# Optimization experiments

Hardware: AMD Instinct MI355X
Metric: run time of the kernel (lower is better)

The kernel has to match this reference:

```python
import jax, jax.numpy as jnp
import numpy as np

E = 8      # num_expert
D = 1024   # d_model
H = 2048   # expert hidden (htoh4 size)
K = 2      # top_k
N = 2048   # tokens (batch*seq)


def setup_inputs() -> dict:
    key = jax.random.key(0)
    ks = jax.random.split(key, 4)
    sc = lambda k, shape, s: jax.random.normal(k, shape, jnp.float32) * s
    return {
        "inp": jax.random.normal(ks[0], (N, D), jnp.float32),
        "Wg": sc(ks[1], (D, E), D ** -0.5),          # NaiveGate linear
        "bg": jnp.zeros((E,), jnp.float32),
        "W1": sc(ks[2], (E, D, H), D ** -0.5),        # per-expert htoh4
        "b1": jnp.zeros((E, H), jnp.float32),
        "W2": sc(ks[3], (E, H, D), H ** -0.5),        # per-expert h4toh
        "b2": jnp.zeros((E, D), jnp.float32),
    }


def reference(inp, Wg, bg, W1, b1, W2, b2):
    # NaiveGate: linear -> top_k logits -> softmax over the k selected logits
    logits = inp @ Wg + bg                              # [N, E]
    top_val, top_idx = jax.lax.top_k(logits, K)         # [N, K]
    gate_score = jax.nn.softmax(top_val, axis=-1)       # [N, K]

    # Expert grouped compute. Reference computes every expert on every token
    # (exact math, no capacity dropping); combine selects the routed ones.
    h = jax.nn.gelu(jnp.einsum('nd,edh->neh', inp, W1) + b1)   # [N, E, H]
    y = jnp.einsum('neh,ehd->ned', h, W2) + b2                 # [N, E, D]

    # Combine: equivalent to bmm(gate_score[N,1,K], x[N,K,D]) after gather.
    comb = jnp.sum(jax.nn.one_hot(top_idx, E, dtype=inp.dtype)
                   * gate_score[..., None], axis=1)            # [N, E]
    return jnp.einsum('ne,ned->nd', comb, y)                   # [N, D]
```

## Files before the change

kernel.cpp:

```cpp
#include <hip/hip_runtime.h>
#include <math.h>

#define N_TOK 2048
#define DM    1024
#define HD    2048
#define NE    8
#define RMAX  5120
#define TMAX  40

typedef short short8 __attribute__((ext_vector_type(8)));
typedef unsigned short u16x8 __attribute__((ext_vector_type(8)));
typedef float f32x4  __attribute__((ext_vector_type(4)));

__device__ inline unsigned short f2b(float f) {
  unsigned int u = __float_as_uint(f);
  return (unsigned short)((u + 0x7FFFu + ((u >> 16) & 1u)) >> 16);
}
__device__ inline float b2f(unsigned short s) {
  return __uint_as_float(((unsigned int)s) << 16);
}
__device__ inline void gload_lds16(const void* g, void* l) {
  __builtin_amdgcn_global_load_lds(
      (const __attribute__((address_space(1))) unsigned int*)g,
      (__attribute__((address_space(3))) unsigned int*)l, 16, 0, 0);
}

__global__ void gate_kernel(const float* __restrict__ inp,
                            const float* __restrict__ Wg,
                            const float* __restrict__ bg,
                            int* __restrict__ top_idx,
                            float* __restrict__ gate_w) {
  int wave = threadIdx.x >> 6;
  int lane = threadIdx.x & 63;
  int n = blockIdx.x * 4 + wave;
  if (n >= N_TOK) return;
  float acc[NE];
#pragma unroll
  for (int e = 0; e < NE; ++e) acc[e] = 0.f;
  const float4* wg4 = reinterpret_cast<const float4*>(Wg);
#pragma unroll
  for (int i = 0; i < DM / 64; ++i) {
    int d = i * 64 + lane;
    float x = inp[n * DM + d];
    float4 w0 = wg4[d * 2 + 0];
    float4 w1 = wg4[d * 2 + 1];
    acc[0] += x * w0.x; acc[1] += x * w0.y; acc[2] += x * w0.z; acc[3] += x * w0.w;
    acc[4] += x * w1.x; acc[5] += x * w1.y; acc[6] += x * w1.z; acc[7] += x * w1.w;
  }
#pragma unroll
  for (int off = 32; off > 0; off >>= 1) {
#pragma unroll
    for (int e = 0; e < NE; ++e) acc[e] += __shfl_xor(acc[e], off);
  }
  if (lane == 0) {
    float v0 = -1e30f, v1 = -1e30f; int i0 = -1, i1 = -1;
#pragma unroll
    for (int e = 0; e < NE; ++e) {
      float v = acc[e] + bg[e];
      if (v > v0)      { v1 = v0; i1 = i0; v0 = v; i0 = e; }
      else if (v > v1) { v1 = v;  i1 = e; }
    }
    float e1 = expf(v1 - v0);
    float s  = 1.f + e1;
    top_idx[n * 2]     = i0;
    top_idx[n * 2 + 1] = i1;
    gate_w[n * 2]      = 1.f / s;
    gate_w[n * 2 + 1]  = e1 / s;
  }
}

__global__ void group_kernel(const int* __restrict__ top_idx,
                             int* __restrict__ token_of,
                             int* __restrict__ inv_g,
                             int* __restrict__ tile_expert,
                             int* __restrict__ tile_row0,
                             int* __restrict__ n_tiles) {
  __shared__ int s_wtot[4];
  int tid = threadIdx.x, lane = tid & 63, wid = tid >> 6;
  int base = 0, tiles = 0;
  for (int e = 0; e < NE; ++e) {
    int cnt = 0;
    for (int c0 = 0; c0 < N_TOK; c0 += 256) {
      int n = c0 + tid;
      int t0 = top_idx[n * 2], t1 = top_idx[n * 2 + 1];
      bool f = (t0 == e) || (t1 == e);
      int k = (t0 == e) ? 0 : 1;
      unsigned long long m = __ballot(f);
      int lp = __popcll(m & ((1ull << lane) - 1ull));
      if (lane == 0) s_wtot[wid] = __popcll(m);
      __syncthreads();
      int wbase = 0;
      for (int w = 0; w < 4; ++w) if (w < wid) wbase += s_wtot[w];
      if (f) {
        int pos = base + cnt + wbase + lp;
        token_of[pos] = n;
        inv_g[n * 2 + k] = pos;
      }
      cnt += s_wtot[0] + s_wtot[1] + s_wtot[2] + s_wtot[3];
      __syncthreads();
    }
    int padded = (cnt + 127) & ~127;
    for (int i = cnt + tid; i < padded; i += 256) token_of[base + i] = -1;
    if (tid == 0) {
      for (int t = 0; t < padded / 128; ++t) {
        tile_expert[tiles + t] = e;
        tile_row0[tiles + t]   = base + t * 128;
      }
    }
    tiles += padded / 128;
    base  += padded;
    __syncthreads();
  }
  if (tid == 0) n_tiles[0] = tiles;
}

__global__ void xcvt_kernel(const float* __restrict__ inp,
                            unsigned short* __restrict__ Xb) {
  int i = (blockIdx.x * 256 + threadIdx.x) * 8;
  float4 a = *(const float4*)(inp + i);
  float4 b = *(const float4*)(inp + i + 4);
  ushort4 pa, pb;
  pa.x = f2b(a.x); pa.y = f2b(a.y); pa.z = f2b(a.z); pa.w = f2b(a.w);
  pb.x = f2b(b.x); pb.y = f2b(b.y); pb.z = f2b(b.z); pb.w = f2b(b.w);
  *(ushort4*)(Xb + i)     = pa;
  *(ushort4*)(Xb + i + 4) = pb;
}

__global__ __launch_bounds__(256) void wcvt_kernel(
    const float* __restrict__ W1, const float* __restrict__ W2,
    unsigned short* __restrict__ W1C, unsigned short* __restrict__ W2C) {
  int z = blockIdx.z;
  const float* src; unsigned short* dst; int K, N;
  if (z < NE) { src = W1 + (size_t)z * DM * HD; dst = W1C + (size_t)z * DM * HD; K = DM; N = HD; }
  else        { src = W2 + (size_t)(z - NE) * HD * DM; dst = W2C + (size_t)(z - NE) * HD * DM; K = HD; N = DM; }
  int n0 = blockIdx.x * 64, k0 = blockIdx.y * 64;
  if (n0 >= N || k0 >= K) return;
  __shared__ float s[64][68];
  int t = threadIdx.x;
  int q = t & 15, r0 = t >> 4;
#pragma unroll
  for (int p = 0; p < 4; ++p) {
    int row = p * 16 + r0;
    float4 v = *(const float4*)(src + (size_t)(k0 + row) * N + n0 + q * 4);
    *(float4*)&s[row][q * 4] = v;
  }
  __syncthreads();
  int n = t & 63;
  int kb0 = t >> 6;
#pragma unroll
  for (int p = 0; p < 2; ++p) {
    int kb = kb0 + p * 4;
    u16x8 o;
#pragma unroll
    for (int i = 0; i < 8; ++i) o[i] = f2b(s[kb * 8 + i][n]);
    *(u16x8*)(dst + ((size_t)(k0 / 8 + kb) * N + n0 + n) * 8) = o;
  }
}

__global__ __launch_bounds__(256) void ffn1_mfma(
    const unsigned short* __restrict__ Xb,
    const unsigned short* __restrict__ W1C,
    const float* __restrict__ b1,
    const unsigned short* __restrict__ zbuf,
    const int* __restrict__ token_of, const int* __restrict__ tile_expert,
    const int* __restrict__ tile_row0, const int* __restrict__ n_tiles,
    unsigned short* __restrict__ Hbuf) {
  if ((int)blockIdx.x >= n_tiles[0]) return;
  int e    = tile_expert[blockIdx.x];
  int row0 = tile_row0[blockIdx.x];
  int h0   = blockIdx.y * 128;
  __shared__ __align__(16) unsigned short Asl[128][32];
  __shared__ __align__(16) unsigned short Bsl[128][32];
  int tid = threadIdx.x, lane = tid & 63;
  int wid = tid >> 6, wr = wid >> 1, wc = wid & 1;
  int l15 = lane & 15, l4 = lane >> 4;

  int tk[2];
#pragma unroll
  for (int q = 0; q < 2; ++q) tk[q] = token_of[row0 + ((tid + q * 256) >> 2)];

  f32x4 acc[4][4] = {};
  const unsigned short* W1e = W1C + (size_t)e * DM * HD;

  for (int kc = 0; kc < DM; kc += 32) {
    __syncthreads();
#pragma unroll
    for (int q = 0; q < 2; ++q) {
      int idx = tid + q * 256;
      const unsigned short* ga = (tk[q] < 0)
          ? zbuf
          : Xb + (size_t)tk[q] * DM + kc + (idx & 3) * 8;
      gload_lds16(ga, (char*)&Asl[0][0] + (size_t)idx * 16);
      const unsigned short* gb =
          W1e + ((size_t)((kc >> 3) + (idx & 3)) * HD + h0 + (idx >> 2)) * 8;
      gload_lds16(gb, (char*)&Bsl[0][0] + (size_t)idx * 16);
    }
    __syncthreads();
    short8 a[4], b[4];
#pragma unroll
    for (int m = 0; m < 4; ++m)
      a[m] = *(const short8*)&Asl[wr * 64 + m * 16 + l15][l4 * 8];
#pragma unroll
    for (int n = 0; n < 4; ++n)
      b[n] = *(const short8*)&Bsl[wc * 64 + n * 16 + l15][l4 * 8];
#pragma unroll
    for (int m = 0; m < 4; ++m)
#pragma unroll
      for (int n = 0; n < 4; ++n)
        acc[m][n] = __builtin_amdgcn_mfma_f32_16x16x32_bf16(a[m], b[n], acc[m][n], 0, 0, 0);
  }

  float bias[4];
#pragma unroll
  for (int n = 0; n < 4; ++n) bias[n] = b1[e * HD + h0 + wc * 64 + n * 16 + l15];
#pragma unroll
  for (int m = 0; m < 4; ++m) {
#pragma unroll
    for (int n = 0; n < 4; ++n) {
      int col = h0 + wc * 64 + n * 16 + l15;
#pragma unroll
      for (int j = 0; j < 4; ++j) {
        int row = row0 + wr * 64 + m * 16 + l4 * 4 + j;
        float x = acc[m][n][j] + bias[n];
        float g = 0.5f * x * (1.f + tanhf(0.7978845608f * (x + 0.044715f * x * x * x)));
        Hbuf[(size_t)row * HD + col] = f2b(g);
      }
    }
  }
}

__global__ __launch_bounds__(256) void ffn2_mfma(
    const unsigned short* __restrict__ Hbuf,
    const unsigned short* __restrict__ W2C,
    const float* __restrict__ b2,
    const int* __restrict__ tile_expert, const int* __restrict__ tile_row0,
    const int* __restrict__ n_tiles,
    unsigned short* __restrict__ Ybuf) {
  if ((int)blockIdx.x >= n_tiles[0]) return;
  int e    = tile_expert[blockIdx.x];
  int row0 = tile_row0[blockIdx.x];
  int d0   = blockIdx.y * 128;
  __shared__ __align__(16) unsigned short Asl[128][32];
  __shared__ __align__(16) unsigned short Bsl[128][32];
  int tid = threadIdx.x, lane = tid & 63;
  int wid = tid >> 6, wr = wid >> 1, wc = wid & 1;
  int l15 = lane & 15, l4 = lane >> 4;

  f32x4 acc[4][4] = {};
  const unsigned short* W2e = W2C + (size_t)e * DM * HD;

  for (int kc = 0; kc < HD; kc += 32) {
    __syncthreads();
#pragma unroll
    for (int q = 0; q < 2; ++q) {
      int idx = tid + q * 256;
      const unsigned short* ga =
          Hbuf + (size_t)(row0 + (idx >> 2)) * HD + kc + (idx & 3) * 8;
      gload_lds16(ga, (char*)&Asl[0][0] + (size_t)idx * 16);
      const unsigned short* gb =
          W2e + ((size_t)((kc >> 3) + (idx & 3)) * DM + d0 + (idx >> 2)) * 8;
      gload_lds16(gb, (char*)&Bsl[0][0] + (size_t)idx * 16);
    }
    __syncthreads();
    short8 a[4], b[4];
#pragma unroll
    for (int m = 0; m < 4; ++m)
      a[m] = *(const short8*)&Asl[wr * 64 + m * 16 + l15][l4 * 8];
#pragma unroll
    for (int n = 0; n < 4; ++n)
      b[n] = *(const short8*)&Bsl[wc * 64 + n * 16 + l15][l4 * 8];
#pragma unroll
    for (int m = 0; m < 4; ++m)
#pragma unroll
      for (int n = 0; n < 4; ++n)
        acc[m][n] = __builtin_amdgcn_mfma_f32_16x16x32_bf16(a[m], b[n], acc[m][n], 0, 0, 0);
  }

  float bias[4];
#pragma unroll
  for (int n = 0; n < 4; ++n) bias[n] = b2[e * DM + d0 + wc * 64 + n * 16 + l15];
#pragma unroll
  for (int m = 0; m < 4; ++m) {
#pragma unroll
    for (int n = 0; n < 4; ++n) {
      int col = d0 + wc * 64 + n * 16 + l15;
#pragma unroll
      for (int j = 0; j < 4; ++j) {
        int row = row0 + wr * 64 + m * 16 + l4 * 4 + j;
        Ybuf[(size_t)row * DM + col] = f2b(acc[m][n][j] + bias[n]);
      }
    }
  }
}

__global__ void combine_kernel(const unsigned short* __restrict__ Ybuf,
                               const int* __restrict__ inv_g,
                               const float* __restrict__ gate_w,
                               float* __restrict__ out) {
  int n = blockIdx.x;
  int r0 = inv_g[n * 2], r1 = inv_g[n * 2 + 1];
  float g0 = gate_w[n * 2], g1 = gate_w[n * 2 + 1];
  int i = threadIdx.x;
  ushort4 a = *(const ushort4*)(Ybuf + (size_t)r0 * DM + i * 4);
  ushort4 b = *(const ushort4*)(Ybuf + (size_t)r1 * DM + i * 4);
  float4 rv;
  rv.x = g0 * b2f(a.x) + g1 * b2f(b.x);
  rv.y = g0 * b2f(a.y) + g1 * b2f(b.y);
  rv.z = g0 * b2f(a.z) + g1 * b2f(b.z);
  rv.w = g0 * b2f(a.w) + g1 * b2f(b.w);
  *(float4*)(out + (size_t)n * DM + i * 4) = rv;
}

extern "C" void kernel_launch(void* const* d_in, const int* in_sizes, int n_in,
                              void* d_out, int out_size, void* d_ws, size_t ws_size,
                              hipStream_t stream) {
  const float* inp = (const float*)d_in[0];
  const float* Wg  = (const float*)d_in[1];
  const float* bg  = (const float*)d_in[2];
  const float* W1  = (const float*)d_in[3];
  const float* b1  = (const float*)d_in[4];
  const float* W2  = (const float*)d_in[5];
  const float* b2  = (const float*)d_in[6];
  float* out = (float*)d_out;

  char* ws = (char*)d_ws;
  size_t off = 0;
  auto alloc = [&](size_t bytes) {
    size_t o = off;
    off = (off + bytes + 255) & ~(size_t)255;
    return o;
  };
  int*   top_idx     = (int*)  (ws + alloc(N_TOK * 2 * sizeof(int)));
  float* gate_w      = (float*)(ws + alloc(N_TOK * 2 * sizeof(float)));
  int*   token_of    = (int*)  (ws + alloc(RMAX * sizeof(int)));
  int*   inv_g       = (int*)  (ws + alloc(N_TOK * 2 * sizeof(int)));
  int*   tile_expert = (int*)  (ws + alloc(TMAX * sizeof(int)));
  int*   tile_row0   = (int*)  (ws + alloc(TMAX * sizeof(int)));
  int*   n_tiles     = (int*)  (ws + alloc(sizeof(int)));
  unsigned short* zbuf = (unsigned short*)(ws + alloc(256));
  unsigned short* Xb   = (unsigned short*)(ws + alloc((size_t)N_TOK * DM * 2));
  unsigned short* W1C  = (unsigned short*)(ws + alloc((size_t)NE * DM * HD * 2));
  unsigned short* W2C  = (unsigned short*)(ws + alloc((size_t)NE * DM * HD * 2));
  unsigned short* Hbuf = (unsigned short*)(ws + alloc((size_t)RMAX * HD * 2));
  unsigned short* Ybuf = (unsigned short*)(ws + alloc((size_t)RMAX * DM * 2));
  (void)ws_size;

  hipMemsetAsync(zbuf, 0, 256, stream);
  gate_kernel<<<N_TOK / 4, 256, 0, stream>>>(inp, Wg, bg, top_idx, gate_w);
  group_kernel<<<1, 256, 0, stream>>>(top_idx, token_of, inv_g,
                                      tile_expert, tile_row0, n_tiles);
  xcvt_kernel<<<(N_TOK * DM) / (256 * 8), 256, 0, stream>>>(inp, Xb);
  wcvt_kernel<<<dim3(32, 32, 2 * NE), 256, 0, stream>>>(W1, W2, W1C, W2C);
  ffn1_mfma<<<dim3(TMAX, HD / 128), 256, 0, stream>>>(
      Xb, W1C, b1, zbuf, token_of, tile_expert, tile_row0, n_tiles, Hbuf);
  ffn2_mfma<<<dim3(TMAX, DM / 128), 256, 0, stream>>>(
      Hbuf, W2C, b2, tile_expert, tile_row0, n_tiles, Ybuf);
  combine_kernel<<<N_TOK, 256, 0, stream>>>(Ybuf, inv_g, gate_w, out);
}
```

Before: 165.6 us.

## Narrow expert GEMM tiles to 128x64, swizzle LDS layout, simplify weight conversion

The FFN1/FFN2 MFMA kernels now use a 64-column output tile instead of 128, doubling the grid to raise occupancy and wave count across the CUs. LDS reads and writes use an XOR swizzle on the 16-byte segments to reduce bank conflicts on the short8 fragment loads. The weight conversion kernel drops its LDS transpose and reads eight strided rows per thread directly, with half-height blocks. Narrower tiles lower the MFMA-to-load ratio and increase total A-tile traffic, since activations are reread twice as often.

Measured after the change: 165.5 us. About the same (-0.1%).

```diff
diff --git a/kernel.cpp b/kernel.cpp
--- a/kernel.cpp
+++ b/kernel.cpp
@@ -133,28 +133,18 @@
   const float* src; unsigned short* dst; int K, N;
   if (z < NE) { src = W1 + (size_t)z * DM * HD; dst = W1C + (size_t)z * DM * HD; K = DM; N = HD; }
   else        { src = W2 + (size_t)(z - NE) * HD * DM; dst = W2C + (size_t)(z - NE) * HD * DM; K = HD; N = DM; }
-  int n0 = blockIdx.x * 64, k0 = blockIdx.y * 64;
+  int n0 = blockIdx.x * 64, k0 = blockIdx.y * 32;
   if (n0 >= N || k0 >= K) return;
-  __shared__ float s[64][68];
   int t = threadIdx.x;
-  int q = t & 15, r0 = t >> 4;
-#pragma unroll
-  for (int p = 0; p < 4; ++p) {
-    int row = p * 16 + r0;
-    float4 v = *(const float4*)(src + (size_t)(k0 + row) * N + n0 + q * 4);
-    *(float4*)&s[row][q * 4] = v;
-  }
-  __syncthreads();
-  int n = t & 63;
-  int kb0 = t >> 6;
-#pragma unroll
-  for (int p = 0; p < 2; ++p) {
-    int kb = kb0 + p * 4;
-    u16x8 o;
-#pragma unroll
-    for (int i = 0; i < 8; ++i) o[i] = f2b(s[kb * 8 + i][n]);
-    *(u16x8*)(dst + ((size_t)(k0 / 8 + kb) * N + n0 + n) * 8) = o;
-  }
+  int n = t & 63, kg = t >> 6;
+  const float* s = src + (size_t)(k0 + kg * 8) * N + n0 + n;
+  float v[8];
+#pragma unroll
+  for (int i = 0; i < 8; ++i) v[i] = s[(size_t)i * N];
+  u16x8 o;
+#pragma unroll
+  for (int i = 0; i < 8; ++i) o[i] = f2b(v[i]);
+  *(u16x8*)(dst + ((size_t)(k0 / 8 + kg) * N + n0 + n) * 8) = o;
 }
 
 __global__ __launch_bounds__(256) void ffn1_mfma(
@@ -168,18 +158,27 @@
   if ((int)blockIdx.x >= n_tiles[0]) return;
   int e    = tile_expert[blockIdx.x];
   int row0 = tile_row0[blockIdx.x];
-  int h0   = blockIdx.y * 128;
+  int h0   = blockIdx.y * 64;
   __shared__ __align__(16) unsigned short Asl[128][32];
-  __shared__ __align__(16) unsigned short Bsl[128][32];
+  __shared__ __align__(16) unsigned short Bsl[64][32];
   int tid = threadIdx.x, lane = tid & 63;
   int wid = tid >> 6, wr = wid >> 1, wc = wid & 1;
   int l15 = lane & 15, l4 = lane >> 4;
-
+  int sw  = (l15 >> 1) & 3;
+
+  int ar[2], asg[2];
   int tk[2];
 #pragma unroll
-  for (int q = 0; q < 2; ++q) tk[q] = token_of[row0 + ((tid + q * 256) >> 2)];
-
-  f32x4 acc[4][4] = {};
+  for (int q = 0; q < 2; ++q) {
+    int idx = tid + q * 256;
+    ar[q]  = idx >> 2;
+    asg[q] = (idx & 3) ^ ((ar[q] >> 1) & 3);
+    tk[q]  = token_of[row0 + ar[q]];
+  }
+  int bc  = tid >> 2;
+  int bsg = (tid & 3) ^ ((bc >> 1) & 3);
+
+  f32x4 acc[4][2] = {};
   const unsigned short* W1e = W1C + (size_t)e * DM * HD;
 
   for (int kc = 0; kc < DM; kc += 32) {
@@ -189,35 +188,41 @@
       int idx = tid + q * 256;
       const unsigned short* ga = (tk[q] < 0)
           ? zbuf
-          : Xb + (size_t)tk[q] * DM + kc + (idx & 3) * 8;
+          : Xb + (size_t)tk[q] * DM + kc + asg[q] * 8;
       gload_lds16(ga, (char*)&Asl[0][0] + (size_t)idx * 16);
+    }
+    {
       const unsigned short* gb =
-          W1e + ((size_t)((kc >> 3) + (idx & 3)) * HD + h0 + (idx >> 2)) * 8;
-      gload_lds16(gb, (char*)&Bsl[0][0] + (size_t)idx * 16);
-    }
-    __syncthreads();
-    short8 a[4], b[4];
+          W1e + ((size_t)((kc >> 3) + bsg) * HD + h0 + bc) * 8;
+      gload_lds16(gb, (char*)&Bsl[0][0] + (size_t)tid * 16);
+    }
+    __syncthreads();
+    short8 a[4], b[2];
+#pragma unroll
+    for (int m = 0; m < 4; ++m) {
+      int R = wr * 64 + m * 16 + l15;
+      a[m] = *(const short8*)((const char*)&Asl[0][0] + R * 64 + ((l4 ^ sw) << 4));
+    }
+#pragma unroll
+    for (int n = 0; n < 2; ++n) {
+      int R = wc * 32 + n * 16 + l15;
+      b[n] = *(const short8*)((const char*)&Bsl[0][0] + R * 64 + ((l4 ^ sw) << 4));
+    }
 #pragma unroll
     for (int m = 0; m < 4; ++m)
-      a[m] = *(const short8*)&Asl[wr * 64 + m * 16 + l15][l4 * 8];
-#pragma unroll
-    for (int n = 0; n < 4; ++n)
-      b[n] = *(const short8*)&Bsl[wc * 64 + n * 16 + l15][l4 * 8];
-#pragma unroll
-    for (int m = 0; m < 4; ++m)
-#pragma unroll
-      for (int n = 0; n < 4; ++n)
+#pragma unroll
+      for (int n = 0; n < 2; ++n)
         acc[m][n] = __builtin_amdgcn_mfma_f32_16x16x32_bf16(a[m], b[n], acc[m][n], 0, 0, 0);
   }
 
-  float bias[4];
-#pragma unroll
-  for (int n = 0; n < 4; ++n) bias[n] = b1[e * HD + h0 + wc * 64 + n * 16 + l15];
+  float bias[2];
+#pragma unroll
+  for (int n = 0; n < 2; ++n) bias[n] = b1[e * HD + h0 + wc * 32 + n * 16 + l15];
 #pragma unroll
   for (int m = 0; m < 4; ++m) {
 #pragma unroll
-    for (int n = 0; n < 4; ++n) {
-      int col = h0 + wc * 64 + n * 16 + l15;
+    for (int n = 0; n < 2; ++n) {
+      int col = h0 + wc * 32 + n * 16 + l15;
 #pragma unroll
       for (int j = 0; j < 4; ++j) {
         int row = row0 + wr * 64 + m * 16 + l4 * 4 + j;
@@ -239,14 +244,25 @@
   if ((int)blockIdx.x >= n_tiles[0]) return;
   int e    = tile_expert[blockIdx.x];
   int row0 = tile_row0[blockIdx.x];
-  int d0   = blockIdx.y * 128;
+  int d0   = blockIdx.y * 64;
   __shared__ __align__(16) unsigned short Asl[128][32];
-  __shared__ __align__(16) unsigned short Bsl[128][32];
+  __shared__ __align__(16) unsigned short Bsl[64][32];
   int tid = threadIdx.x, lane = tid & 63;
   int wid = tid >> 6, wr = wid >> 1, wc = wid & 1;
   int l15 = lane & 15, l4 = lane >> 4;
-
-  f32x4 acc[4][4] = {};
+  int sw  = (l15 >> 1) & 3;
+
+  int ar[2], asg[2];
+#pragma unroll
+  for (int q = 0; q < 2; ++q) {
+    int idx = tid + q * 256;
+    ar[q]  = idx >> 2;
+    asg[q] = (idx & 3) ^ ((ar[q] >> 1) & 3);
+  }
+  int bc  = tid >> 2;
+  int bsg = (tid & 3) ^ ((bc >> 1) & 3);
+
+  f32x4 acc[4][2] = {};
   const unsigned short* W2e = W2C + (size_t)e * DM * HD;
 
   for (int kc = 0; kc < HD; kc += 32) {
@@ -255,35 +271,41 @@
     for (int q = 0; q < 2; ++q) {
       int idx = tid + q * 256;
       const unsigned short* ga =
-          Hbuf + (size_t)(row0 + (idx >> 2)) * HD + kc + (idx & 3) * 8;
+          Hbuf + (size_t)(row0 + ar[q]) * HD + kc + asg[q] * 8;
       gload_lds16(ga, (char*)&Asl[0][0] + (size_t)idx * 16);
+    }
+    {
       const unsigned short* gb =
-          W2e + ((size_t)((kc >> 3) + (idx & 3)) * DM + d0 + (idx >> 2)) * 8;
-      gload_lds16(gb, (char*)&Bsl[0][0] + (size_t)idx * 16);
-    }
-    __syncthreads();
-    short8 a[4], b[4];
+          W2e + ((size_t)((kc >> 3) + bsg) * DM + d0 + bc) * 8;
+      gload_lds16(gb, (char*)&Bsl[0][0] + (size_t)tid * 16);
+    }
+    __syncthreads();
+    short8 a[4], b[2];
+#pragma unroll
+    for (int m = 0; m < 4; ++m) {
+      int R = wr * 64 + m * 16 + l15;
+      a[m] = *(const short8*)((const char*)&Asl[0][0] + R * 64 + ((l4 ^ sw) << 4));
+    }
+#pragma unroll
+    for (int n = 0; n < 2; ++n) {
+      int R = wc * 32 + n * 16 + l15;
+      b[n] = *(const short8*)((const char*)&Bsl[0][0] + R * 64 + ((l4 ^ sw) << 4));
+    }
 #pragma unroll
     for (int m = 0; m < 4; ++m)
-      a[m] = *(const short8*)&Asl[wr * 64 + m * 16 + l15][l4 * 8];
-#pragma unroll
-    for (int n = 0; n < 4; ++n)
-      b[n] = *(const short8*)&Bsl[wc * 64 + n * 16 + l15][l4 * 8];
-#pragma unroll
-    for (int m = 0; m < 4; ++m)
-#pragma unroll
-      for (int n = 0; n < 4; ++n)
+#pragma unroll
+      for (int n = 0; n < 2; ++n)
         acc[m][n] = __builtin_amdgcn_mfma_f32_16x16x32_bf16(a[m], b[n], acc[m][n], 0, 0, 0);
   }
 
-  float bias[4];
-#pragma unroll
-  for (int n = 0; n < 4; ++n) bias[n] = b2[e * DM + d0 + wc * 64 + n * 16 + l15];
+  float bias[2];
+#pragma unroll
+  for (int n = 0; n < 2; ++n) bias[n] = b2[e * DM + d0 + wc * 32 + n * 16 + l15];
 #pragma unroll
   for (int m = 0; m < 4; ++m) {
 #pragma unroll
-    for (int n = 0; n < 4; ++n) {
-      int col = d0 + wc * 64 + n * 16 + l15;
+    for (int n = 0; n < 2; ++n) {
+      int col = d0 + wc * 32 + n * 16 + l15;
 #pragma unroll
       for (int j = 0; j < 4; ++j) {
         int row = row0 + wr * 64 + m * 16 + l4 * 4 + j;
@@ -350,10 +372,10 @@
   group_kernel<<<1, 256, 0, stream>>>(top_idx, token_of, inv_g,
                                       tile_expert, tile_row0, n_tiles);
   xcvt_kernel<<<(N_TOK * DM) / (256 * 8), 256, 0, stream>>>(inp, Xb);
-  wcvt_kernel<<<dim3(32, 32, 2 * NE), 256, 0, stream>>>(W1, W2, W1C, W2C);
-  ffn1_mfma<<<dim3(TMAX, HD / 128), 256, 0, stream>>>(
+  wcvt_kernel<<<dim3(32, 64, 2 * NE), 256, 0, stream>>>(W1, W2, W1C, W2C);
+  ffn1_mfma<<<dim3(TMAX, HD / 64), 256, 0, stream>>>(
       Xb, W1C, b1, zbuf, token_of, tile_expert, tile_row0, n_tiles, Hbuf);
-  ffn2_mfma<<<dim3(TMAX, DM / 128), 256, 0, stream>>>(
+  ffn2_mfma<<<dim3(TMAX, DM / 64), 256, 0, stream>>>(
       Hbuf, W2C, b2, tile_expert, tile_row0, n_tiles, Ybuf);
   combine_kernel<<<N_TOK, 256, 0, stream>>>(Ybuf, inv_g, gate_w, out);
 }
```
